# Performance work log

Hardware: AMD Instinct MI355X
Metric: run time of the kernel (lower is better)

The kernel has to match this reference:

```python
import jax, jax.numpy as jnp
import numpy as np

B, X_DIM, Z_DIM, K = 16384, 784, 64, 64
LOG2PI = 1.8378770664093453


def setup_inputs() -> dict:
    key = jax.random.key(0)
    ks = jax.random.split(key, 8)
    pi_raw = jax.random.uniform(ks[1], (B, K), dtype=jnp.float32) + 1e-3
    pi = pi_raw / jnp.sum(pi_raw, axis=1, keepdims=True)
    return {
        "x": jax.random.normal(ks[0], (B, X_DIM), dtype=jnp.float32),
        "pi": pi,
        "qz_mu": jax.random.normal(ks[2], (B, Z_DIM), dtype=jnp.float32),
        "qz_logsigma": 0.5 * jax.random.normal(ks[3], (B, Z_DIM), dtype=jnp.float32),
        "eps": jax.random.normal(ks[4], (B, Z_DIM), dtype=jnp.float32),
        "pz_y_mu": jax.random.normal(ks[5], (K, Z_DIM), dtype=jnp.float32),
        "pz_y_logsigma": jnp.zeros((K, Z_DIM), dtype=jnp.float32),  # log(init_sigma=1.0)
        "W_dec": jax.random.normal(ks[6], (Z_DIM, X_DIM), dtype=jnp.float32) / np.sqrt(Z_DIM),
        "b_dec": jnp.zeros((X_DIM,), dtype=jnp.float32),
    }


def reference(x, pi, qz_mu, qz_logsigma, eps, pz_y_mu, pz_y_logsigma, W_dec, b_dec):
    # GMMVAE.elbo with num_samples=1; rsample reparameterized with fixed eps.
    qs = jnp.exp(qz_logsigma)                      # [B, z]
    z = qz_mu + qs * eps                           # [B, z]

    # log p(x | z): unit-variance Gaussian likelihood with linear decoder
    mean = z @ W_dec + b_dec                       # [B, x]
    log_px_z = jnp.sum(-0.5 * (x - mean) ** 2 - 0.5 * LOG2PI)

    # py_z: vectorized over all k components (fuses the original Python loop)
    ps = jnp.exp(pz_y_logsigma)                    # [k, z]
    diff = z[:, None, :] - pz_y_mu[None, :, :]     # [B, k, z]
    comp_lp = jnp.sum(-0.5 * (diff / ps[None]) ** 2 - pz_y_logsigma[None] - 0.5 * LOG2PI, axis=-1)  # [B, k]
    log_pi = jnp.log(pi)
    pzy = comp_lp + log_pi                         # [B, k]
    log_py_z = pzy - jax.scipy.special.logsumexp(pzy, axis=1, keepdims=True)
    probs = jnp.exp(log_py_z)                      # [B, k]

    # kl_y = sum_b KL(Cat(py_z) || Cat(pi))
    kl_y = jnp.sum(probs * (log_py_z - log_pi))

    # kl_z = sum_b sum_k probs[b,k] * KL(N(qz_mu, qs) || N(mu_k, ps_k)).sum(z)
    mdiff = qz_mu[:, None, :] - pz_y_mu[None, :, :]  # [B, k, z]
    klz_bk = jnp.sum(
        pz_y_logsigma[None] - qz_logsigma[:, None, :]
        + (qs[:, None, :] ** 2 + mdiff ** 2) / (2.0 * ps[None] ** 2)
        - 0.5,
        axis=-1,
    )                                              # [B, k]
    kl_z = jnp.sum(probs * klz_bk)

    elbo = (log_px_z - kl_y - kl_z) / x.shape[0]
    return elbo
```

## Files before the change

### kernel.cpp

```cpp
#include <hip/hip_runtime.h>

#define NB 16384
#define XD 784
#define ZD 64
#define KK 64
#define LOG2PI_F 1.8378770664093453f
#define LDA 72

typedef __attribute__((ext_vector_type(8))) short short8;
typedef __attribute__((ext_vector_type(4))) float floatx4;


__device__ __forceinline__ float wave_sum(float x) {
    #pragma unroll
    for (int o = 32; o > 0; o >>= 1) x += __shfl_xor(x, o, 64);
    return x;
}

__device__ __forceinline__ unsigned short f2bf(float f) {
    unsigned u = __float_as_uint(f);
    unsigned r = (u + 0x7FFF + ((u >> 16) & 1)) >> 16;
    return (unsigned short)r;
}

__device__ __forceinline__ unsigned int pack2(float a, float b) {
    return (unsigned int)f2bf(a) | ((unsigned int)f2bf(b) << 16);
}

__global__ __launch_bounds__(256) void prep_kernel(
    const float* __restrict__ W, unsigned short* __restrict__ Wt, double* __restrict__ acc)
{
    if (blockIdx.x == 0 && threadIdx.x < 3) acc[threadIdx.x] = 0.0;
    int idx = blockIdx.x * 256 + threadIdx.x;
    if (idx < ZD * XD) {
        int k = idx / XD;
        int n = idx - k * XD;
        Wt[n * ZD + k] = f2bf(W[idx]);
    }
}

__global__ __launch_bounds__(256) void mixture_mfma_kernel(
    const float* __restrict__ pi, const float* __restrict__ qmu,
    const float* __restrict__ qls, const float* __restrict__ eps,
    const float* __restrict__ pmu_g, const float* __restrict__ plog_g,
    double* __restrict__ acc)
{
    __shared__ unsigned short Az2[64 * LDA];
    __shared__ unsigned short Azm[64 * LDA];
    __shared__ unsigned short Aq2[64 * LDA];
    __shared__ unsigned short Aqm[64 * LDA];
    __shared__ unsigned short Bi2[64 * LDA];
    __shared__ unsigned short Bm1[64 * LDA];
    __shared__ float Ck_s[KK], Sk_s[KK], Gk_s[KK], sq_s[64];
    __shared__ float r1[4], r2[4];

    const int tid  = threadIdx.x;
    const int row0 = blockIdx.x * 64;

    {
        const int r  = tid >> 2;
        const int q  = tid & 3;
        const int v0 = q * 16;
        const int gb = (row0 + r) * 64 + v0;
        float4 mu4[4], ls4[4], ep4[4];
        #pragma unroll
        for (int i = 0; i < 4; ++i) {
            mu4[i] = *(const float4*)&qmu[gb + 4 * i];
            ls4[i] = *(const float4*)&qls[gb + 4 * i];
            ep4[i] = *(const float4*)&eps[gb + 4 * i];
        }
        float sls = 0.f;
        unsigned int* pz2 = (unsigned int*)&Az2[r * LDA + v0];
        unsigned int* pzm = (unsigned int*)&Azm[r * LDA + v0];
        unsigned int* pq2 = (unsigned int*)&Aq2[r * LDA + v0];
        unsigned int* pqm = (unsigned int*)&Aqm[r * LDA + v0];
        #pragma unroll
        for (int i = 0; i < 4; ++i) {
            float m0[4] = {mu4[i].x, mu4[i].y, mu4[i].z, mu4[i].w};
            float l0[4] = {ls4[i].x, ls4[i].y, ls4[i].z, ls4[i].w};
            float e0[4] = {ep4[i].x, ep4[i].y, ep4[i].z, ep4[i].w};
            float z[4], q2[4];
            #pragma unroll
            for (int j = 0; j < 4; ++j) {
                float qs = __expf(l0[j]);
                z[j]  = fmaf(qs, e0[j], m0[j]);
                q2[j] = fmaf(m0[j], m0[j], qs * qs);
                sls += l0[j];
            }
            pz2[i * 2 + 0] = pack2(z[0] * z[0], z[1] * z[1]);
            pz2[i * 2 + 1] = pack2(z[2] * z[2], z[3] * z[3]);
            pzm[i * 2 + 0] = pack2(-2.f * z[0], -2.f * z[1]);
            pzm[i * 2 + 1] = pack2(-2.f * z[2], -2.f * z[3]);
            pq2[i * 2 + 0] = pack2(q2[0], q2[1]);
            pq2[i * 2 + 1] = pack2(q2[2], q2[3]);
            pqm[i * 2 + 0] = pack2(-2.f * m0[0], -2.f * m0[1]);
            pqm[i * 2 + 1] = pack2(-2.f * m0[2], -2.f * m0[3]);
        }
        sls += __shfl_xor(sls, 1, 64);
        sls += __shfl_xor(sls, 2, 64);
        if (q == 0) sq_s[r] = sls;
    }

    {
        const int k  = tid >> 2;
        const int q  = tid & 3;
        const int v0 = q * 16;
        const int gb = k * 64 + v0;
        float s = 0.f, g = 0.f;
        unsigned int* pi2 = (unsigned int*)&Bi2[k * LDA + v0];
        unsigned int* pm1 = (unsigned int*)&Bm1[k * LDA + v0];
        #pragma unroll
        for (int i = 0; i < 4; ++i) {
            float4 mu4 = *(const float4*)&pmu_g[gb + 4 * i];
            float4 lg4 = *(const float4*)&plog_g[gb + 4 * i];
            float m0[4] = {mu4.x, mu4.y, mu4.z, mu4.w};
            float l0[4] = {lg4.x, lg4.y, lg4.z, lg4.w};
            float i2v[4], m1v[4];
            #pragma unroll
            for (int j = 0; j < 4; ++j) {
                float i2 = 0.5f * __expf(-2.f * l0[j]);
                i2v[j] = i2;
                m1v[j] = m0[j] * i2;
                g = fmaf(m0[j] * m0[j], i2, g);
                s += l0[j];
            }
            pi2[i * 2 + 0] = pack2(i2v[0], i2v[1]);
            pi2[i * 2 + 1] = pack2(i2v[2], i2v[3]);
            pm1[i * 2 + 0] = pack2(m1v[0], m1v[1]);
            pm1[i * 2 + 1] = pack2(m1v[2], m1v[3]);
        }
        s += __shfl_xor(s, 1, 64);
        s += __shfl_xor(s, 2, 64);
        g += __shfl_xor(g, 1, 64);
        g += __shfl_xor(g, 2, 64);
        if (q == 0) {
            Sk_s[k] = s;
            Gk_s[k] = g;
            Ck_s[k] = -s - 32.0f * LOG2PI_F;
        }
    }
    __syncthreads();

    const int lane  = tid & 63;
    const int wid   = tid >> 6;
    const int mm    = lane & 15;
    const int quad  = lane >> 4;
    const int rbase = wid * 16;

    const short8 az2_0 = *(const short8*)&Az2[(rbase + mm) * LDA + quad * 8];
    const short8 az2_1 = *(const short8*)&Az2[(rbase + mm) * LDA + 32 + quad * 8];
    const short8 azm_0 = *(const short8*)&Azm[(rbase + mm) * LDA + quad * 8];
    const short8 azm_1 = *(const short8*)&Azm[(rbase + mm) * LDA + 32 + quad * 8];
    const short8 aq2_0 = *(const short8*)&Aq2[(rbase + mm) * LDA + quad * 8];
    const short8 aq2_1 = *(const short8*)&Aq2[(rbase + mm) * LDA + 32 + quad * 8];
    const short8 aqm_0 = *(const short8*)&Aqm[(rbase + mm) * LDA + quad * 8];
    const short8 aqm_1 = *(const short8*)&Aqm[(rbase + mm) * LDA + 32 + quad * 8];

    floatx4 acc_a[4], acc_c[4];
    #pragma unroll
    for (int t = 0; t < 4; ++t) {
        const int kr = t * 16 + mm;
        const short8 bi0 = *(const short8*)&Bi2[kr * LDA + quad * 8];
        const short8 bi1 = *(const short8*)&Bi2[kr * LDA + 32 + quad * 8];
        const short8 bm0 = *(const short8*)&Bm1[kr * LDA + quad * 8];
        const short8 bm1 = *(const short8*)&Bm1[kr * LDA + 32 + quad * 8];
        floatx4 ca = {0.f, 0.f, 0.f, 0.f};
        ca = __builtin_amdgcn_mfma_f32_16x16x32_bf16(az2_0, bi0, ca, 0, 0, 0);
        ca = __builtin_amdgcn_mfma_f32_16x16x32_bf16(az2_1, bi1, ca, 0, 0, 0);
        ca = __builtin_amdgcn_mfma_f32_16x16x32_bf16(azm_0, bm0, ca, 0, 0, 0);
        ca = __builtin_amdgcn_mfma_f32_16x16x32_bf16(azm_1, bm1, ca, 0, 0, 0);
        acc_a[t] = ca;
        floatx4 cc = {0.f, 0.f, 0.f, 0.f};
        cc = __builtin_amdgcn_mfma_f32_16x16x32_bf16(aq2_0, bi0, cc, 0, 0, 0);
        cc = __builtin_amdgcn_mfma_f32_16x16x32_bf16(aq2_1, bi1, cc, 0, 0, 0);
        cc = __builtin_amdgcn_mfma_f32_16x16x32_bf16(aqm_0, bm0, cc, 0, 0, 0);
        cc = __builtin_amdgcn_mfma_f32_16x16x32_bf16(aqm_1, bm1, cc, 0, 0, 0);
        acc_c[t] = cc;
    }

    float comp[4][4], pz[4][4];
    #pragma unroll
    for (int t = 0; t < 4; ++t) {
        const int k = t * 16 + mm;
        const float ck = Ck_s[k], gk = Gk_s[k];
        #pragma unroll
        for (int r = 0; r < 4; ++r) {
            const int gb = row0 + rbase + quad * 4 + r;
            comp[t][r] = ck - (acc_a[t][r] + gk);
            pz[t][r] = comp[t][r] + __logf(pi[gb * 64 + k]);
        }
    }

    float kly = 0.f, klz = 0.f;
    #pragma unroll
    for (int r = 0; r < 4; ++r) {
        float mx = fmaxf(fmaxf(pz[0][r], pz[1][r]), fmaxf(pz[2][r], pz[3][r]));
        #pragma unroll
        for (int o = 1; o <= 8; o <<= 1) mx = fmaxf(mx, __shfl_xor(mx, o, 64));
        float e[4];
        float s = 0.f;
        #pragma unroll
        for (int t = 0; t < 4; ++t) { e[t] = __expf(pz[t][r] - mx); s += e[t]; }
        #pragma unroll
        for (int o = 1; o <= 8; o <<= 1) s += __shfl_xor(s, o, 64);
        const float lse = mx + __logf(s);
        const float inv = __frcp_rn(s);
        const float sql = sq_s[rbase + quad * 4 + r];
        #pragma unroll
        for (int t = 0; t < 4; ++t) {
            const int k = t * 16 + mm;
            const float p = e[t] * inv;
            kly = fmaf(p, comp[t][r] - lse, kly);
            const float cv = acc_c[t][r] + Gk_s[k];
            klz = fmaf(p, Sk_s[k] - sql + cv - 32.0f, klz);
        }
    }

    kly = wave_sum(kly);
    klz = wave_sum(klz);
    if (lane == 0) { r1[wid] = kly; r2[wid] = klz; }
    __syncthreads();
    if (tid == 0) {
        atomicAdd(&acc[1], (double)(r1[0] + r1[1] + r1[2] + r1[3]));
        atomicAdd(&acc[2], (double)(r2[0] + r2[1] + r2[2] + r2[3]));
    }
}

__global__ __launch_bounds__(256) void decoder_mfma_kernel(
    const float* __restrict__ x, const float* __restrict__ qmu,
    const float* __restrict__ qls, const float* __restrict__ eps,
    const unsigned short* __restrict__ Wt, const float* __restrict__ bd,
    double* __restrict__ acc)
{
    __shared__ unsigned short zt[16 * 64];
    __shared__ float rs[4];
    const int tid  = threadIdx.x;
    const int row0 = blockIdx.x * 16;

    for (int i = tid; i < 16 * 64; i += 256) {
        int g = row0 * 64 + i;
        float z = fmaf(__expf(qls[g]), eps[g], qmu[g]);
        zt[i] = f2bf(z);
    }
    __syncthreads();

    const int lane = tid & 63;
    const int wid  = tid >> 6;
    const int m    = lane & 15;
    const int quad = lane >> 4;

    const short8 af0 = *(const short8*)&zt[m * 64 + quad * 8];
    const short8 af1 = *(const short8*)&zt[m * 64 + 32 + quad * 8];

    float accl = 0.f;
    #pragma unroll 1
    for (int t = wid; t < 49; t += 4) {
        const int col = t * 16 + m;
        float x0 = x[(row0 + quad * 4 + 0) * XD + col];
        float x1 = x[(row0 + quad * 4 + 1) * XD + col];
        float x2 = x[(row0 + quad * 4 + 2) * XD + col];
        float x3 = x[(row0 + quad * 4 + 3) * XD + col];
        float b0 = bd[col];
        const short8 bf0 = *(const short8*)&Wt[col * 64 + quad * 8];
        const short8 bf1 = *(const short8*)&Wt[col * 64 + 32 + quad * 8];
        floatx4 c = {0.f, 0.f, 0.f, 0.f};
        c = __builtin_amdgcn_mfma_f32_16x16x32_bf16(af0, bf0, c, 0, 0, 0);
        c = __builtin_amdgcn_mfma_f32_16x16x32_bf16(af1, bf1, c, 0, 0, 0);
        float d0 = x0 - (c[0] + b0);
        float d1 = x1 - (c[1] + b0);
        float d2 = x2 - (c[2] + b0);
        float d3 = x3 - (c[3] + b0);
        accl = fmaf(d0, d0, accl);
        accl = fmaf(d1, d1, accl);
        accl = fmaf(d2, d2, accl);
        accl = fmaf(d3, d3, accl);
    }

    float s = wave_sum(accl);
    if (lane == 0) rs[wid] = s;
    __syncthreads();
    if (tid == 0)
        atomicAdd(&acc[0], (double)(-0.5f * (rs[0] + rs[1] + rs[2] + rs[3])));
}

__global__ void finalize_kernel(const double* __restrict__ acc, float* __restrict__ out) {
    if (threadIdx.x == 0) {
        double lpx = acc[0] - 0.5 * 1.8378770664093453 * (double)NB * (double)XD;
        double elbo = (lpx - acc[1] - acc[2]) / (double)NB;
        out[0] = (float)elbo;
    }
}

extern "C" void kernel_launch(void* const* d_in, const int* in_sizes, int n_in,
                              void* d_out, int out_size, void* d_ws, size_t ws_size,
                              hipStream_t stream) {
    const float* x    = (const float*)d_in[0];
    const float* pi   = (const float*)d_in[1];
    const float* qmu  = (const float*)d_in[2];
    const float* qls  = (const float*)d_in[3];
    const float* eps  = (const float*)d_in[4];
    const float* pmu  = (const float*)d_in[5];
    const float* plog = (const float*)d_in[6];
    const float* W    = (const float*)d_in[7];
    const float* bd   = (const float*)d_in[8];
    float* out = (float*)d_out;
    double* acc = (double*)d_ws;
    unsigned short* Wt = (unsigned short*)((char*)d_ws + 256);

    prep_kernel<<<(ZD * XD + 255) / 256, 256, 0, stream>>>(W, Wt, acc);
    mixture_mfma_kernel<<<NB / 64, 256, 0, stream>>>(pi, qmu, qls, eps, pmu, plog, acc);
    decoder_mfma_kernel<<<NB / 16, 256, 0, stream>>>(x, qmu, qls, eps, Wt, bd, acc);
    finalize_kernel<<<1, 64, 0, stream>>>(acc, out);
}
```

Before: 136.8 us.

## Prefetch decoder loads one iteration ahead and replace atomics with per-block partials

```diff
diff --git a/kernel.cpp b/kernel.cpp
--- a/kernel.cpp
+++ b/kernel.cpp
@@ -28,9 +28,8 @@
 }
 
 __global__ __launch_bounds__(256) void prep_kernel(
-    const float* __restrict__ W, unsigned short* __restrict__ Wt, double* __restrict__ acc)
+    const float* __restrict__ W, unsigned short* __restrict__ Wt)
 {
-    if (blockIdx.x == 0 && threadIdx.x < 3) acc[threadIdx.x] = 0.0;
     int idx = blockIdx.x * 256 + threadIdx.x;
     if (idx < ZD * XD) {
         int k = idx / XD;
@@ -43,7 +42,7 @@
     const float* __restrict__ pi, const float* __restrict__ qmu,
     const float* __restrict__ qls, const float* __restrict__ eps,
     const float* __restrict__ pmu_g, const float* __restrict__ plog_g,
-    double* __restrict__ acc)
+    float* __restrict__ kly_p, float* __restrict__ klz_p)
 {
     __shared__ unsigned short Az2[64 * LDA];
     __shared__ unsigned short Azm[64 * LDA];
@@ -221,8 +220,8 @@
     if (lane == 0) { r1[wid] = kly; r2[wid] = klz; }
     __syncthreads();
     if (tid == 0) {
-        atomicAdd(&acc[1], (double)(r1[0] + r1[1] + r1[2] + r1[3]));
-        atomicAdd(&acc[2], (double)(r2[0] + r2[1] + r2[2] + r2[3]));
+        kly_p[blockIdx.x] = r1[0] + r1[1] + r1[2] + r1[3];
+        klz_p[blockIdx.x] = r2[0] + r2[1] + r2[2] + r2[3];
     }
 }
 
@@ -230,7 +229,7 @@
     const float* __restrict__ x, const float* __restrict__ qmu,
     const float* __restrict__ qls, const float* __restrict__ eps,
     const unsigned short* __restrict__ Wt, const float* __restrict__ bd,
-    double* __restrict__ acc)
+    float* __restrict__ dec_p)
 {
     __shared__ unsigned short zt[16 * 64];
     __shared__ float rs[4];
@@ -252,24 +251,44 @@
     const short8 af0 = *(const short8*)&zt[m * 64 + quad * 8];
     const short8 af1 = *(const short8*)&zt[m * 64 + 32 + quad * 8];
 
+    const int xrow = (row0 + quad * 4) * XD;
+
+    float xa0, xa1, xa2, xa3, bb;
+    short8 w0, w1;
+    {
+        const int col = wid * 16 + m;
+        xa0 = x[xrow + 0 * XD + col];
+        xa1 = x[xrow + 1 * XD + col];
+        xa2 = x[xrow + 2 * XD + col];
+        xa3 = x[xrow + 3 * XD + col];
+        bb  = bd[col];
+        w0  = *(const short8*)&Wt[col * 64 + quad * 8];
+        w1  = *(const short8*)&Wt[col * 64 + 32 + quad * 8];
+    }
+
     float accl = 0.f;
     #pragma unroll 1
     for (int t = wid; t < 49; t += 4) {
-        const int col = t * 16 + m;
-        float x0 = x[(row0 + quad * 4 + 0) * XD + col];
-        float x1 = x[(row0 + quad * 4 + 1) * XD + col];
-        float x2 = x[(row0 + quad * 4 + 2) * XD + col];
-        float x3 = x[(row0 + quad * 4 + 3) * XD + col];
-        float b0 = bd[col];
-        const short8 bf0 = *(const short8*)&Wt[col * 64 + quad * 8];
-        const short8 bf1 = *(const short8*)&Wt[col * 64 + 32 + quad * 8];
+        const float cx0 = xa0, cx1 = xa1, cx2 = xa2, cx3 = xa3, cb = bb;
+        const short8 cw0 = w0, cw1 = w1;
+        const int tn = t + 4;
+        if (tn < 49) {
+            const int col = tn * 16 + m;
+            xa0 = x[xrow + 0 * XD + col];
+            xa1 = x[xrow + 1 * XD + col];
+            xa2 = x[xrow + 2 * XD + col];
+            xa3 = x[xrow + 3 * XD + col];
+            bb  = bd[col];
+            w0  = *(const short8*)&Wt[col * 64 + quad * 8];
+            w1  = *(const short8*)&Wt[col * 64 + 32 + quad * 8];
+        }
         floatx4 c = {0.f, 0.f, 0.f, 0.f};
-        c = __builtin_amdgcn_mfma_f32_16x16x32_bf16(af0, bf0, c, 0, 0, 0);
-        c = __builtin_amdgcn_mfma_f32_16x16x32_bf16(af1, bf1, c, 0, 0, 0);
-        float d0 = x0 - (c[0] + b0);
-        float d1 = x1 - (c[1] + b0);
-        float d2 = x2 - (c[2] + b0);
-        float d3 = x3 - (c[3] + b0);
+        c = __builtin_amdgcn_mfma_f32_16x16x32_bf16(af0, cw0, c, 0, 0, 0);
+        c = __builtin_amdgcn_mfma_f32_16x16x32_bf16(af1, cw1, c, 0, 0, 0);
+        float d0 = cx0 - (c[0] + cb);
+        float d1 = cx1 - (c[1] + cb);
+        float d2 = cx2 - (c[2] + cb);
+        float d3 = cx3 - (c[3] + cb);
         accl = fmaf(d0, d0, accl);
         accl = fmaf(d1, d1, accl);
         accl = fmaf(d2, d2, accl);
@@ -280,14 +299,33 @@
     if (lane == 0) rs[wid] = s;
     __syncthreads();
     if (tid == 0)
-        atomicAdd(&acc[0], (double)(-0.5f * (rs[0] + rs[1] + rs[2] + rs[3])));
-}
-
-__global__ void finalize_kernel(const double* __restrict__ acc, float* __restrict__ out) {
-    if (threadIdx.x == 0) {
-        double lpx = acc[0] - 0.5 * 1.8378770664093453 * (double)NB * (double)XD;
-        double elbo = (lpx - acc[1] - acc[2]) / (double)NB;
-        out[0] = (float)elbo;
+        dec_p[blockIdx.x] = -0.5f * (rs[0] + rs[1] + rs[2] + rs[3]);
+}
+
+__global__ __launch_bounds__(256) void finalize_kernel(
+    const float* __restrict__ dec_p, const float* __restrict__ kly_p,
+    const float* __restrict__ klz_p, float* __restrict__ out)
+{
+    __shared__ double s0[256], s1[256], s2[256];
+    const int tid = threadIdx.x;
+    double a0 = 0.0, a1 = 0.0, a2 = 0.0;
+    for (int i = tid; i < 1024; i += 256) a0 += (double)dec_p[i];
+    a1 = (double)kly_p[tid];
+    a2 = (double)klz_p[tid];
+    s0[tid] = a0; s1[tid] = a1; s2[tid] = a2;
+    __syncthreads();
+    #pragma unroll
+    for (int off = 128; off > 0; off >>= 1) {
+        if (tid < off) {
+            s0[tid] += s0[tid + off];
+            s1[tid] += s1[tid + off];
+            s2[tid] += s2[tid + off];
+        }
+        __syncthreads();
+    }
+    if (tid == 0) {
+        double lpx = s0[0] - 0.5 * 1.8378770664093453 * (double)NB * (double)XD;
+        out[0] = (float)((lpx - s1[0] - s2[0]) / (double)NB);
     }
 }
 
@@ -304,11 +342,15 @@
     const float* W    = (const float*)d_in[7];
     const float* bd   = (const float*)d_in[8];
     float* out = (float*)d_out;
-    double* acc = (double*)d_ws;
-    unsigned short* Wt = (unsigned short*)((char*)d_ws + 256);
-
-    prep_kernel<<<(ZD * XD + 255) / 256, 256, 0, stream>>>(W, Wt, acc);
-    mixture_mfma_kernel<<<NB / 64, 256, 0, stream>>>(pi, qmu, qls, eps, pmu, plog, acc);
-    decoder_mfma_kernel<<<NB / 16, 256, 0, stream>>>(x, qmu, qls, eps, Wt, bd, acc);
-    finalize_kernel<<<1, 64, 0, stream>>>(acc, out);
-}
+
+    unsigned short* Wt = (unsigned short*)d_ws;
+    float* fp    = (float*)((char*)d_ws + 100352);
+    float* dec_p = fp;
+    float* kly_p = fp + 1024;
+    float* klz_p = fp + 1280;
+
+    prep_kernel<<<(ZD * XD + 255) / 256, 256, 0, stream>>>(W, Wt);
+    mixture_mfma_kernel<<<NB / 64, 256, 0, stream>>>(pi, qmu, qls, eps, pmu, plog, kly_p, klz_p);
+    decoder_mfma_kernel<<<NB / 16, 256, 0, stream>>>(x, qmu, qls, eps, Wt, bd, dec_p);
+    finalize_kernel<<<1, 256, 0, stream>>>(dec_p, kly_p, klz_p, out);
+}
```

Result: faster. 127.2 us (-7.0%).
